# Optimization experiments

Measured on AMD Instinct MI355X. Metric: run time of the kernel, lower is better.

The kernel has to match this reference:

```python
import jax, jax.numpy as jnp
import numpy as np

ANCHOR = jnp.array([[116.0, 90.0], [156.0, 198.0], [373.0, 326.0]], dtype=jnp.float32)
CLS = 80  # classes per anchor


def setup_inputs() -> dict:
    key = jax.random.key(0)
    N, H, W = 8, 128, 128
    C = ANCHOR.shape[0] * (5 + CLS)  # 255
    x = jax.random.normal(key, (N, C, H, W), dtype=jnp.float32)
    return {"x": x}


def reference(x):
    N, C, H, W = x.shape
    A = ANCHOR.shape[0]
    cls = CLS
    # [N, A, 5+cls, H, W]
    xr = x.reshape(N, A, 5 + cls, H, W)

    gx = jnp.arange(W, dtype=x.dtype)            # broadcasts along W (last axis)
    gy = jnp.arange(H, dtype=x.dtype)[:, None]   # broadcasts along H

    bx = jax.nn.sigmoid(xr[:, :, 0]) + gx        # sigmoid(tx) + cx
    by = jax.nn.sigmoid(xr[:, :, 1]) + gy        # sigmoid(ty) + cy
    # NOTE: original code writes exp(tw/th) then immediately OVERWRITES with raw*anchor
    bw = xr[:, :, 2] * ANCHOR[None, :, 0, None, None]
    bh = xr[:, :, 3] * ANCHOR[None, :, 1, None, None]

    # score = class logits * raw objectness (no sigmoid), shape [N, A, cls, H, W]
    score = xr[:, :, 5:] * xr[:, :, 4:5]
    # original torch.max/argmax reduce over the full [N, cls] slice per pixel,
    # flat index order = n*cls + c; result broadcast to all batch elements.
    s = jnp.transpose(score, (1, 0, 2, 3, 4)).reshape(A, N * cls, H, W)
    smax = jnp.broadcast_to(jnp.max(s, axis=1)[None], (N, A, H, W))
    sarg = jnp.broadcast_to(jnp.argmax(s, axis=1).astype(x.dtype)[None], (N, A, H, W))

    out = jnp.stack([bx, by, bw, bh, smax, sarg], axis=2)  # [N, A, 6, H, W]
    return out.reshape(N, A * 6, H, W)
```

## Files before the change

### kernel.cpp

```cpp
#include <hip/hip_runtime.h>


#define NN   8
#define AA   3
#define CLSN 80
#define HW   16384
#define CH   255

__global__ __launch_bounds__(256)
void anchor_kernel(const float* __restrict__ x, float* __restrict__ out) {
    const int tid = threadIdx.x;
    const int p   = tid & 31;
    const int n   = tid >> 5;
    const int pix = blockIdx.x * 32 + p;
    const int h   = pix >> 7;
    const int w   = pix & 127;

    const float anchw[AA] = {116.f, 156.f, 373.f};
    const float anchh[AA] = { 90.f, 198.f, 326.f};

    const int nbase = n * (CH * HW) + pix;

    __shared__ float s_val[AA][NN][32];
    __shared__ int   s_idx[AA][NN][32];

    #pragma unroll
    for (int a = 0; a < AA; ++a) {
        const int abase = nbase + (a * 85) * HW;
        const float tx  = x[abase + 0 * HW];
        const float ty  = x[abase + 1 * HW];
        const float tw  = x[abase + 2 * HW];
        const float th  = x[abase + 3 * HW];
        const float obj = x[abase + 4 * HW];

        const float bx = 1.0f / (1.0f + __expf(-tx)) + (float)w;
        const float by = 1.0f / (1.0f + __expf(-ty)) + (float)h;
        const float bw = tw * anchw[a];
        const float bh = th * anchh[a];

        const int obase = (n * 18 + a * 6) * HW + pix;
        out[obase + 0 * HW] = bx;
        out[obase + 1 * HW] = by;
        out[obase + 2 * HW] = bw;
        out[obase + 3 * HW] = bh;

        float best = -__builtin_inff();
        int   bidx = n * CLSN;
        #pragma unroll 8
        for (int c = 0; c < CLSN; ++c) {
            const float v = x[abase + (5 + c) * HW] * obj;
            if (v > best) { best = v; bidx = n * CLSN + c; }
        }
        s_val[a][n][p] = best;
        s_idx[a][n][p] = bidx;
    }
    __syncthreads();

    #pragma unroll
    for (int a = 0; a < AA; ++a) {
        float best = s_val[a][0][p];
        int   bidx = s_idx[a][0][p];
        #pragma unroll
        for (int nn = 1; nn < NN; ++nn) {
            const float v  = s_val[a][nn][p];
            const int   id = s_idx[a][nn][p];
            if (v > best || (v == best && id < bidx)) { best = v; bidx = id; }
        }
        const int obase = (n * 18 + a * 6) * HW + pix;
        out[obase + 4 * HW] = best;
        out[obase + 5 * HW] = (float)bidx;
    }
}

extern "C" void kernel_launch(void* const* d_in, const int* in_sizes, int n_in,
                              void* d_out, int out_size, void* d_ws, size_t ws_size,
                              hipStream_t stream) {
    const float* x = (const float*)d_in[0];
    float* out = (float*)d_out;
    dim3 grid(HW / 32);
    dim3 block(256);
    hipLaunchKernelGGL(anchor_kernel, grid, block, 0, stream, x, out);
}
```

Measured before the change: 28.62 us.

## Vectorize loads to float4 per thread and split class scan across two halves

Each thread now handles four adjacent pixels with float4 loads and stores, and the 80-class argmax is split into two 40-class halves run by separate thread groups. The blocks cover 64 pixels, which halves the grid, and the final reduction merges 16 partial results per pixel through shared memory. The goal is fewer, wider memory transactions and more parallelism per pixel on the bandwidth-bound class scan. In exchange the 4-wide independent chains raise register use and the shared-memory merge does more work.

Result: slower. 36.88 us (+28.9%).

```diff
diff --git a/kernel.cpp b/kernel.cpp
--- a/kernel.cpp
+++ b/kernel.cpp
@@ -7,68 +7,103 @@
 #define HW   16384
 #define CH   255
 
+__device__ __forceinline__ float sigf(float v) {
+    return 1.0f / (1.0f + __expf(-v));
+}
+
 __global__ __launch_bounds__(256)
-void anchor_kernel(const float* __restrict__ x, float* __restrict__ out) {
-    const int tid = threadIdx.x;
-    const int p   = tid & 31;
-    const int n   = tid >> 5;
-    const int pix = blockIdx.x * 32 + p;
-    const int h   = pix >> 7;
-    const int w   = pix & 127;
+void anchor_kernel_v2(const float* __restrict__ x, float* __restrict__ out) {
+    const int tid   = threadIdx.x;
+    const int p     = tid & 15;
+    const int n     = (tid >> 4) & 7;
+    const int chalf = tid >> 7;
+    const int pix   = blockIdx.x * 64 + p * 4;
+    const int h     = pix >> 7;
+    const int w0    = pix & 127;
 
     const float anchw[AA] = {116.f, 156.f, 373.f};
     const float anchh[AA] = { 90.f, 198.f, 326.f};
 
     const int nbase = n * (CH * HW) + pix;
 
-    __shared__ float s_val[AA][NN][32];
-    __shared__ int   s_idx[AA][NN][32];
+    __shared__ float4 s_val[AA][NN][2][16];
+    __shared__ int4   s_idx[AA][NN][2][16];
 
     #pragma unroll
     for (int a = 0; a < AA; ++a) {
         const int abase = nbase + (a * 85) * HW;
-        const float tx  = x[abase + 0 * HW];
-        const float ty  = x[abase + 1 * HW];
-        const float tw  = x[abase + 2 * HW];
-        const float th  = x[abase + 3 * HW];
-        const float obj = x[abase + 4 * HW];
+        const float4 obj = *(const float4*)(x + abase + 4 * HW);
 
-        const float bx = 1.0f / (1.0f + __expf(-tx)) + (float)w;
-        const float by = 1.0f / (1.0f + __expf(-ty)) + (float)h;
-        const float bw = tw * anchw[a];
-        const float bh = th * anchh[a];
+        if (chalf == 0) {
+            const float4 tx = *(const float4*)(x + abase + 0 * HW);
+            const float4 ty = *(const float4*)(x + abase + 1 * HW);
+            const float4 tw = *(const float4*)(x + abase + 2 * HW);
+            const float4 th = *(const float4*)(x + abase + 3 * HW);
+            float4 bx, by, bw, bh;
+            bx.x = sigf(tx.x) + (float)(w0 + 0);
+            bx.y = sigf(tx.y) + (float)(w0 + 1);
+            bx.z = sigf(tx.z) + (float)(w0 + 2);
+            bx.w = sigf(tx.w) + (float)(w0 + 3);
+            const float fh = (float)h;
+            by.x = sigf(ty.x) + fh;  by.y = sigf(ty.y) + fh;
+            by.z = sigf(ty.z) + fh;  by.w = sigf(ty.w) + fh;
+            bw.x = tw.x * anchw[a];  bw.y = tw.y * anchw[a];
+            bw.z = tw.z * anchw[a];  bw.w = tw.w * anchw[a];
+            bh.x = th.x * anchh[a];  bh.y = th.y * anchh[a];
+            bh.z = th.z * anchh[a];  bh.w = th.w * anchh[a];
+            const int obase = (n * 18 + a * 6) * HW + pix;
+            *(float4*)(out + obase + 0 * HW) = bx;
+            *(float4*)(out + obase + 1 * HW) = by;
+            *(float4*)(out + obase + 2 * HW) = bw;
+            *(float4*)(out + obase + 3 * HW) = bh;
+        }
 
-        const int obase = (n * 18 + a * 6) * HW + pix;
-        out[obase + 0 * HW] = bx;
-        out[obase + 1 * HW] = by;
-        out[obase + 2 * HW] = bw;
-        out[obase + 3 * HW] = bh;
-
-        float best = -__builtin_inff();
-        int   bidx = n * CLSN;
+        float4 best = make_float4(-__builtin_inff(), -__builtin_inff(),
+                                  -__builtin_inff(), -__builtin_inff());
+        int4 bidx = make_int4(0x7fffffff, 0x7fffffff, 0x7fffffff, 0x7fffffff);
+        const int cbeg = 5 + chalf * 40;
+        const int ibeg = n * CLSN + chalf * 40;
         #pragma unroll 8
-        for (int c = 0; c < CLSN; ++c) {
-            const float v = x[abase + (5 + c) * HW] * obj;
-            if (v > best) { best = v; bidx = n * CLSN + c; }
+        for (int c = 0; c < 40; ++c) {
+            float4 v = *(const float4*)(x + abase + (cbeg + c) * HW);
+            v.x *= obj.x; v.y *= obj.y; v.z *= obj.z; v.w *= obj.w;
+            const int id = ibeg + c;
+            if (v.x > best.x) { best.x = v.x; bidx.x = id; }
+            if (v.y > best.y) { best.y = v.y; bidx.y = id; }
+            if (v.z > best.z) { best.z = v.z; bidx.z = id; }
+            if (v.w > best.w) { best.w = v.w; bidx.w = id; }
         }
-        s_val[a][n][p] = best;
-        s_idx[a][n][p] = bidx;
+        s_val[a][n][chalf][p] = best;
+        s_idx[a][n][chalf][p] = bidx;
     }
     __syncthreads();
 
     #pragma unroll
     for (int a = 0; a < AA; ++a) {
-        float best = s_val[a][0][p];
-        int   bidx = s_idx[a][0][p];
+        float4 best = make_float4(-__builtin_inff(), -__builtin_inff(),
+                                  -__builtin_inff(), -__builtin_inff());
+        int4 bidx = make_int4(0x7fffffff, 0x7fffffff, 0x7fffffff, 0x7fffffff);
         #pragma unroll
-        for (int nn = 1; nn < NN; ++nn) {
-            const float v  = s_val[a][nn][p];
-            const int   id = s_idx[a][nn][p];
-            if (v > best || (v == best && id < bidx)) { best = v; bidx = id; }
+        for (int nn = 0; nn < NN; ++nn) {
+            #pragma unroll
+            for (int ch = 0; ch < 2; ++ch) {
+                const float4 v  = s_val[a][nn][ch][p];
+                const int4   id = s_idx[a][nn][ch][p];
+                if (v.x > best.x || (v.x == best.x && id.x < bidx.x)) { best.x = v.x; bidx.x = id.x; }
+                if (v.y > best.y || (v.y == best.y && id.y < bidx.y)) { best.y = v.y; bidx.y = id.y; }
+                if (v.z > best.z || (v.z == best.z && id.z < bidx.z)) { best.z = v.z; bidx.z = id.z; }
+                if (v.w > best.w || (v.w == best.w && id.w < bidx.w)) { best.w = v.w; bidx.w = id.w; }
+            }
         }
         const int obase = (n * 18 + a * 6) * HW + pix;
-        out[obase + 4 * HW] = best;
-        out[obase + 5 * HW] = (float)bidx;
+        if (chalf == 0) {
+            *(float4*)(out + obase + 4 * HW) = best;
+        } else {
+            float4 f;
+            f.x = (float)bidx.x; f.y = (float)bidx.y;
+            f.z = (float)bidx.z; f.w = (float)bidx.w;
+            *(float4*)(out + obase + 5 * HW) = f;
+        }
     }
 }
 
@@ -77,7 +112,7 @@
                               hipStream_t stream) {
     const float* x = (const float*)d_in[0];
     float* out = (float*)d_out;
-    dim3 grid(HW / 32);
+    dim3 grid(HW / 64);
     dim3 block(256);
-    hipLaunchKernelGGL(anchor_kernel, grid, block, 0, stream, x, out);
+    hipLaunchKernelGGL(anchor_kernel_v2, grid, block, 0, stream, x, out);
 }
```

## Split anchors across blocks and widen pixel tile to full wavefront

Applied to the files above, without the earlier changes.

Each block now handles a single anchor and 64 pixels (one full wavefront per batch element) instead of looping over all three anchors for 32 pixels. The grid grows to 768 blocks of 512 threads, so there are more independent memory streams in flight and reads are 256-byte coalesced per wavefront rather than 128-byte half-wave accesses. This trades the per-thread serial anchor loop for more parallelism and smaller shared-memory arrays per block. The argmax tie-break initial index also changes to a sentinel value.

Measured after the change: 27.61 us. 1.04x faster.

```diff
diff --git a/kernel.cpp b/kernel.cpp
--- a/kernel.cpp
+++ b/kernel.cpp
@@ -7,69 +7,63 @@
 #define HW   16384
 #define CH   255
 
-__global__ __launch_bounds__(256)
-void anchor_kernel(const float* __restrict__ x, float* __restrict__ out) {
-    const int tid = threadIdx.x;
-    const int p   = tid & 31;
-    const int n   = tid >> 5;
-    const int pix = blockIdx.x * 32 + p;
+__device__ __forceinline__ float sigf(float v) {
+    return 1.0f / (1.0f + __expf(-v));
+}
+
+__global__ __launch_bounds__(512, 6)
+void anchor_kernel_v4(const float* __restrict__ x, float* __restrict__ out) {
+    const int lane = threadIdx.x & 63;
+    const int n    = threadIdx.x >> 6;
+
+    const int bid = blockIdx.x;
+    const int a   = bid >> 8;
+    const int pg  = bid & 255;
+    const int pix = pg * 64 + lane;
     const int h   = pix >> 7;
     const int w   = pix & 127;
 
     const float anchw[AA] = {116.f, 156.f, 373.f};
     const float anchh[AA] = { 90.f, 198.f, 326.f};
 
-    const int nbase = n * (CH * HW) + pix;
+    const int abase = n * (CH * HW) + (a * 85) * HW + pix;
 
-    __shared__ float s_val[AA][NN][32];
-    __shared__ int   s_idx[AA][NN][32];
+    const float tx  = x[abase + 0 * HW];
+    const float ty  = x[abase + 1 * HW];
+    const float tw  = x[abase + 2 * HW];
+    const float th  = x[abase + 3 * HW];
+    const float obj = x[abase + 4 * HW];
 
-    #pragma unroll
-    for (int a = 0; a < AA; ++a) {
-        const int abase = nbase + (a * 85) * HW;
-        const float tx  = x[abase + 0 * HW];
-        const float ty  = x[abase + 1 * HW];
-        const float tw  = x[abase + 2 * HW];
-        const float th  = x[abase + 3 * HW];
-        const float obj = x[abase + 4 * HW];
+    const int obase = (n * 18 + a * 6) * HW + pix;
+    out[obase + 0 * HW] = sigf(tx) + (float)w;
+    out[obase + 1 * HW] = sigf(ty) + (float)h;
+    out[obase + 2 * HW] = tw * anchw[a];
+    out[obase + 3 * HW] = th * anchh[a];
 
-        const float bx = 1.0f / (1.0f + __expf(-tx)) + (float)w;
-        const float by = 1.0f / (1.0f + __expf(-ty)) + (float)h;
-        const float bw = tw * anchw[a];
-        const float bh = th * anchh[a];
+    float best = -__builtin_inff();
+    int   bidx = 0x7fffffff;
+    #pragma unroll 8
+    for (int c = 0; c < CLSN; ++c) {
+        const float v = x[abase + (5 + c) * HW] * obj;
+        if (v > best) { best = v; bidx = n * CLSN + c; }
+    }
 
-        const int obase = (n * 18 + a * 6) * HW + pix;
-        out[obase + 0 * HW] = bx;
-        out[obase + 1 * HW] = by;
-        out[obase + 2 * HW] = bw;
-        out[obase + 3 * HW] = bh;
-
-        float best = -__builtin_inff();
-        int   bidx = n * CLSN;
-        #pragma unroll 8
-        for (int c = 0; c < CLSN; ++c) {
-            const float v = x[abase + (5 + c) * HW] * obj;
-            if (v > best) { best = v; bidx = n * CLSN + c; }
-        }
-        s_val[a][n][p] = best;
-        s_idx[a][n][p] = bidx;
-    }
+    __shared__ float s_val[NN][64];
+    __shared__ int   s_idx[NN][64];
+    s_val[n][lane] = best;
+    s_idx[n][lane] = bidx;
     __syncthreads();
 
+    float fbest = s_val[0][lane];
+    int   fidx  = s_idx[0][lane];
     #pragma unroll
-    for (int a = 0; a < AA; ++a) {
-        float best = s_val[a][0][p];
-        int   bidx = s_idx[a][0][p];
-        #pragma unroll
-        for (int nn = 1; nn < NN; ++nn) {
-            const float v  = s_val[a][nn][p];
-            const int   id = s_idx[a][nn][p];
-            if (v > best || (v == best && id < bidx)) { best = v; bidx = id; }
-        }
-        const int obase = (n * 18 + a * 6) * HW + pix;
-        out[obase + 4 * HW] = best;
-        out[obase + 5 * HW] = (float)bidx;
+    for (int nn = 1; nn < NN; ++nn) {
+        const float v  = s_val[nn][lane];
+        const int   id = s_idx[nn][lane];
+        if (v > fbest || (v == fbest && id < fidx)) { fbest = v; fidx = id; }
     }
+    out[obase + 4 * HW] = fbest;
+    out[obase + 5 * HW] = (float)fidx;
 }
 
 extern "C" void kernel_launch(void* const* d_in, const int* in_sizes, int n_in,
@@ -77,7 +71,7 @@
                               hipStream_t stream) {
     const float* x = (const float*)d_in[0];
     float* out = (float*)d_out;
-    dim3 grid(HW / 32);
-    dim3 block(256);
-    hipLaunchKernelGGL(anchor_kernel, grid, block, 0, stream, x, out);
+    dim3 grid(AA * 256);
+    dim3 block(512);
+    hipLaunchKernelGGL(anchor_kernel_v4, grid, block, 0, stream, x, out);
 }
```
